# Optimization experiments

Hardware: AMD Instinct MI355X
Metric: run time of the kernel (lower is better)

Reference implementation:

```python
import jax, jax.numpy as jnp
import numpy as np

B, DIN, E, H, V = 1024, 512, 512, 1024, 4096
MAX_LEN = 32  # max_len=33 with force_eos=True -> 32 decode steps


def setup_inputs() -> dict:
    key = jax.random.key(0)
    ks = jax.random.split(key, 12)
    def u(k, shape, fan_in):
        s = 1.0 / np.sqrt(fan_in)
        return jax.random.uniform(k, shape, jnp.float32, -s, s)
    return {
        "x": jax.random.normal(ks[0], (B, DIN), jnp.float32),
        "W_agent": u(ks[1], (DIN, H), DIN),
        "b_agent": u(ks[2], (H,), DIN),
        "sos_embedding": 0.01 * jax.random.normal(ks[3], (E,), jnp.float32),
        "emb": jax.random.normal(ks[4], (V, E), jnp.float32),
        "W_ih": u(ks[5], (E, H), H),
        "W_hh": u(ks[6], (H, H), H),
        "b_ih": u(ks[7], (H,), H),
        "b_hh": u(ks[8], (H,), H),
        "W_out": u(ks[9], (H, V), H),
        "b_out": u(ks[10], (V,), H),
    }


def reference(x, W_agent, b_agent, sos_embedding, emb, W_ih, W_hh, b_ih, b_hh, W_out, b_out):
    h0 = x @ W_agent + b_agent                      # agent(x): [B, H]
    inp0 = jnp.broadcast_to(sos_embedding, (x.shape[0], E))

    def step(carry, _):
        inp, h = carry
        h = jnp.tanh(inp @ W_ih + h @ W_hh + b_ih + b_hh)   # RNNCell
        logp = jax.nn.log_softmax(h @ W_out + b_out, axis=1)  # [B, V]
        tok = jnp.argmax(logp, axis=1)                      # eval-mode sample
        lp = jnp.take_along_axis(logp, tok[:, None], axis=1)[:, 0]
        ent = -jnp.sum(jnp.exp(logp) * logp, axis=1)
        return (emb[tok], h), (tok, lp, ent)

    (_, _), (seq, lps, ents) = jax.lax.scan(step, (inp0, h0), None, length=MAX_LEN)
    seq = seq.T        # [B, MAX_LEN]
    lps = lps.T
    ents = ents.T
    # force_eos: append zero column
    zf = jnp.zeros((seq.shape[0], 1), jnp.float32)
    sequence = jnp.concatenate([seq, zf.astype(seq.dtype)], axis=1)
    logits = jnp.concatenate([lps, zf], axis=1)
    entropy = jnp.concatenate([ents, zf], axis=1)
    return sequence, logits, entropy
```

## Files before the change

kernel.cpp:

```cpp
#include <hip/hip_runtime.h>
#include <math.h>

#define B_   1024
#define DIN  512
#define EMB  512
#define H_   1024
#define V_   4096
#define TSTEPS 32
#define LEN  33

typedef __attribute__((ext_vector_type(8))) short short8_t;
typedef __attribute__((ext_vector_type(4))) float f32x4;

#define AH_P  131072
#define AI_P  65536
#define B3_P  196608

__device__ inline unsigned short bf16_rne(float f) {
  unsigned u = __builtin_bit_cast(unsigned, f);
  u += 0x7FFFu + ((u >> 16) & 1u);
  return (unsigned short)(u >> 16);
}
__device__ inline float bf16_to_f(unsigned short h) {
  unsigned u = ((unsigned)h) << 16;
  return __builtin_bit_cast(float, u);
}
struct S3 { short a, b, c; };
__device__ inline S3 split3(float w) {
  unsigned short h0 = bf16_rne(w);  float r1 = w - bf16_to_f(h0);
  unsigned short h1 = bf16_rne(r1); float r2 = r1 - bf16_to_f(h1);
  S3 r; r.a = (short)h0; r.b = (short)h1; r.c = (short)bf16_rne(r2);
  return r;
}

#define T2MERGE(M1,I1,M2,I2, o1,oi1,o2,oi2)                              \
  if (o1 > M1 || (o1 == M1 && oi1 < I1)) {                               \
    float _n2; int _ni2;                                                 \
    if (M1 > o2 || (M1 == o2 && I1 < oi2)) { _n2 = M1; _ni2 = I1; }      \
    else { _n2 = o2; _ni2 = oi2; }                                       \
    M1 = o1; I1 = oi1; M2 = _n2; I2 = _ni2;                              \
  } else if (o1 > M2 || (o1 == M2 && oi1 < I2)) { M2 = o1; I2 = oi1; }

#define GBT 4
#define GKC 256
__global__ __launch_bounds__(256) void k_gemm(
    float* __restrict__ out,
    const float* __restrict__ A1, int K1, const float* __restrict__ W1,
    const float* __restrict__ A2, int K2, const float* __restrict__ W2,
    const float* __restrict__ b1, const float* __restrict__ b2,
    int do_tanh)
{
  const int N = H_;
  __shared__ float sA[GBT][GKC];
  const int tid = threadIdx.x;
  const int bid = blockIdx.x;
  const int colb = (bid & 7) >> 1;
  const int rowb = ((bid >> 3) << 1) | (bid & 1);
  const int rb  = rowb * GBT;
  const int col = colb * 256 + tid;

  float acc[GBT];
  float bias = b1[col] + (b2 ? b2[col] : 0.0f);
#pragma unroll
  for (int r = 0; r < GBT; ++r) acc[r] = bias;

  const int nch = (K1 + K2) / GKC;
  for (int c = 0; c < nch; ++c) {
    const int kb = c * GKC;
    const float* A; const float* W; int k0, strideA;
    if (kb < K1) { A = A1; W = W1; k0 = kb;      strideA = K1; }
    else         { A = A2; W = W2; k0 = kb - K1; strideA = K2; }
    __syncthreads();
    {
      int r = tid >> 6, kk = (tid & 63) << 2;
      *(float4*)&sA[r][kk] = *(const float4*)(A + (size_t)(rb + r) * strideA + k0 + kk);
    }
    __syncthreads();
    const float* Wp = W + (size_t)k0 * N + col;
#pragma unroll 4
    for (int k = 0; k < GKC; k += 4) {
      float4 a0 = *(const float4*)&sA[0][k];
      float4 a1 = *(const float4*)&sA[1][k];
      float4 a2 = *(const float4*)&sA[2][k];
      float4 a3 = *(const float4*)&sA[3][k];
      float w0 = Wp[(size_t)k * N];
      float w1 = Wp[(size_t)(k + 1) * N];
      float w2 = Wp[(size_t)(k + 2) * N];
      float w3 = Wp[(size_t)(k + 3) * N];
      acc[0] = fmaf(a0.x, w0, acc[0]); acc[1] = fmaf(a1.x, w0, acc[1]);
      acc[2] = fmaf(a2.x, w0, acc[2]); acc[3] = fmaf(a3.x, w0, acc[3]);
      acc[0] = fmaf(a0.y, w1, acc[0]); acc[1] = fmaf(a1.y, w1, acc[1]);
      acc[2] = fmaf(a2.y, w1, acc[2]); acc[3] = fmaf(a3.y, w1, acc[3]);
      acc[0] = fmaf(a0.z, w2, acc[0]); acc[1] = fmaf(a1.z, w2, acc[1]);
      acc[2] = fmaf(a2.z, w2, acc[2]); acc[3] = fmaf(a3.z, w2, acc[3]);
      acc[0] = fmaf(a0.w, w3, acc[0]); acc[1] = fmaf(a1.w, w3, acc[1]);
      acc[2] = fmaf(a2.w, w3, acc[2]); acc[3] = fmaf(a3.w, w3, acc[3]);
    }
  }
#pragma unroll
  for (int r = 0; r < GBT; ++r) {
    float v = acc[r];
    if (do_tanh) v = tanhf(v);
    out[(size_t)(rb + r) * N + col] = v;
  }
}

__global__ __launch_bounds__(256) void k_prepack(
    const float* __restrict__ W, unsigned short* __restrict__ Bp)
{
  int t = blockIdx.x * 256 + threadIdx.x;
  int lane = t & 63;
  int ntg  = (t >> 6) & 255;
  int ks   = t >> 14;
  int col  = ntg * 16 + (lane & 15);
  int krow = ks * 32 + ((lane >> 4) << 3);
  short8_t hv;
#pragma unroll
  for (int j = 0; j < 8; ++j) {
    float w = W[(size_t)(krow + j) * V_ + col];
    hv[j] = (short)bf16_rne(w);
  }
  size_t base = ((size_t)ks * 256 + ntg) * 64 + lane;
  ((short8_t*)Bp)[base] = hv;
}

__global__ __launch_bounds__(256) void k_packW3(
    const float* __restrict__ Wih, const float* __restrict__ Whh,
    unsigned short* __restrict__ BU)
{
  int t = blockIdx.x * 256 + threadIdx.x;
  int lane = t & 63;
  int ntg  = (t >> 6) & 63;
  int ks   = t >> 12;
  int col  = ntg * 16 + (lane & 15);
  int krow = ks * 32 + ((lane >> 4) << 3);
  short8_t p0, p1, p2;
#pragma unroll
  for (int j = 0; j < 8; ++j) {
    int kr = krow + j;
    float w = (kr < DIN) ? Wih[(size_t)kr * H_ + col]
                         : Whh[(size_t)(kr - DIN) * H_ + col];
    S3 s = split3(w);
    p0[j] = s.a; p1[j] = s.b; p2[j] = s.c;
  }
  short8_t* o = (short8_t*)BU;
  size_t base = ((size_t)ks * 64 + ntg) * 64 + lane;
  o[base] = p0; o[base + B3_P] = p1; o[base + 2 * B3_P] = p2;
}

__global__ __launch_bounds__(256) void k_wtrans(
    const float* __restrict__ W, float* __restrict__ WT)
{
  __shared__ float tile[64][65];
  int kb = (blockIdx.x & 15) * 64;
  int vb = (blockIdx.x >> 4) * 64;
  int t = threadIdx.x;
  {
    int vv = t & 63, k0 = (t >> 6) * 16;
    for (int j = 0; j < 16; ++j)
      tile[k0 + j][vv] = W[(size_t)(kb + k0 + j) * V_ + vb + vv];
  }
  __syncthreads();
  {
    int kk = t & 63, v0 = (t >> 6) * 16;
    for (int j = 0; j < 16; ++j)
      WT[(size_t)(vb + v0 + j) * H_ + kb + kk] = tile[kk][v0 + j];
  }
}

__global__ __launch_bounds__(256) void k_packh(
    const float* __restrict__ h, unsigned short* __restrict__ AU)
{
  int t = blockIdx.x * 256 + threadIdx.x;
  int r = t >> 7, q = t & 127;
  int ks = q >> 2, kg = q & 3;
  int lanep = (r & 15) + (kg << 4);
  int rt = r >> 4;
  const float* src = h + (size_t)r * H_ + q * 8;
  float4 f0 = *(const float4*)src;
  float4 f1 = *(const float4*)(src + 4);
  float f[8] = {f0.x, f0.y, f0.z, f0.w, f1.x, f1.y, f1.z, f1.w};
  short8_t p0, p1, p2;
#pragma unroll
  for (int j = 0; j < 8; ++j) {
    S3 s = split3(f[j]);
    p0[j] = s.a; p1[j] = s.b; p2[j] = s.c;
  }
  short8_t* o = (short8_t*)AU;
  size_t base = (size_t)rt * 2048 + (size_t)ks * 64 + lanep;
  o[base] = p0; o[base + AH_P] = p1; o[base + 2 * AH_P] = p2;
}

__global__ __launch_bounds__(256) void k_sos3(
    const float* __restrict__ sos, unsigned short* __restrict__ AU)
{
  int wid = threadIdx.x >> 6, lane = threadIdx.x & 63;
  int row = blockIdx.x * 4 + wid;
  const float* src = sos + lane * 8;
  float4 f0 = *(const float4*)src;
  float4 f1 = *(const float4*)(src + 4);
  float f[8] = {f0.x, f0.y, f0.z, f0.w, f1.x, f1.y, f1.z, f1.w};
  short8_t p0, p1, p2;
#pragma unroll
  for (int j = 0; j < 8; ++j) {
    S3 s = split3(f[j]);
    p0[j] = s.a; p1[j] = s.b; p2[j] = s.c;
  }
  int ks = lane >> 2, kg = lane & 3;
  int lanep = (row & 15) + (kg << 4);
  int rt = row >> 4;
  short8_t* o = (short8_t*)AU;
  size_t base = (size_t)rt * 1024 + (size_t)ks * 64 + lanep;
  o[base] = p0; o[base + AI_P] = p1; o[base + 2 * AI_P] = p2;
}

__global__ __launch_bounds__(512) void k_rnn(
    const unsigned short* __restrict__ AinpU, const unsigned short* __restrict__ AhU,
    const unsigned short* __restrict__ Bw3U,
    const float* __restrict__ b1, const float* __restrict__ b2,
    float* __restrict__ hout, unsigned short* __restrict__ AhOutU)
{
  __shared__ float sh[64][65];
  const short8_t* Ainp = (const short8_t*)AinpU;
  const short8_t* Ah   = (const short8_t*)AhU;
  const short8_t* Bw3  = (const short8_t*)Bw3U;

  const int bid  = blockIdx.x;
  const int colb = ((bid & 7) << 1) | ((bid >> 3) & 1);
  const int rowb = bid >> 4;
  const int tid  = threadIdx.x, lane = tid & 63, wid = tid >> 6;
  const int wm = (wid >> 1) & 1, wn = wid & 1, kh = wid >> 2;
  const int l15 = lane & 15, lg = lane >> 4;

  f32x4 acc[2][2];
#pragma unroll
  for (int rt = 0; rt < 2; ++rt)
#pragma unroll
    for (int nt = 0; nt < 2; ++nt) {
      int col = colb * 64 + wn * 32 + nt * 16 + l15;
      float b = (kh == 0) ? (b1[col] + b2[col]) : 0.0f;
      acc[rt][nt] = (f32x4){b, b, b, b};
    }

  const int rt0 = rowb * 4 + wm * 2;
  const int ng0 = colb * 4 + wn * 2;
  const int ks0 = kh * 24;

#define RNN_LOAD(A_, B_, KS)                                                   \
  {                                                                            \
    int _ks = (KS);                                                            \
    if (_ks < 16) {                                                            \
      _Pragma("unroll") for (int rt = 0; rt < 2; ++rt)                         \
        _Pragma("unroll") for (int p = 0; p < 3; ++p)                          \
          A_[rt][p] = Ainp[(size_t)p * AI_P + (size_t)(rt0 + rt) * 1024 +      \
                           (size_t)_ks * 64 + lane];                           \
    } else {                                                                   \
      int _h = _ks - 16;                                                       \
      _Pragma("unroll") for (int rt = 0; rt < 2; ++rt)                         \
        _Pragma("unroll") for (int p = 0; p < 3; ++p)                          \
          A_[rt][p] = Ah[(size_t)p * AH_P + (size_t)(rt0 + rt) * 2048 +        \
                         (size_t)_h * 64 + lane];                              \
    }                                                                          \
    _Pragma("unroll") for (int nt = 0; nt < 2; ++nt)                           \
      _Pragma("unroll") for (int p = 0; p < 3; ++p)                            \
        B_[nt][p] = Bw3[(size_t)p * B3_P + (size_t)_ks * 4096 +                \
                        (size_t)(ng0 + nt) * 64 + lane];                       \
  }

  short8_t a[2][3], bb[2][3];
  RNN_LOAD(a, bb, ks0)
#pragma unroll
  for (int i = 0; i < 24; ++i) {
    short8_t an[2][3], bn[2][3];
    if (i < 23) RNN_LOAD(an, bn, ks0 + i + 1)
#pragma unroll
    for (int rt = 0; rt < 2; ++rt)
#pragma unroll
      for (int nt = 0; nt < 2; ++nt) {
        acc[rt][nt] = __builtin_amdgcn_mfma_f32_16x16x32_bf16(a[rt][0], bb[nt][0], acc[rt][nt], 0, 0, 0);
        acc[rt][nt] = __builtin_amdgcn_mfma_f32_16x16x32_bf16(a[rt][0], bb[nt][1], acc[rt][nt], 0, 0, 0);
        acc[rt][nt] = __builtin_amdgcn_mfma_f32_16x16x32_bf16(a[rt][1], bb[nt][0], acc[rt][nt], 0, 0, 0);
        acc[rt][nt] = __builtin_amdgcn_mfma_f32_16x16x32_bf16(a[rt][1], bb[nt][1], acc[rt][nt], 0, 0, 0);
        acc[rt][nt] = __builtin_amdgcn_mfma_f32_16x16x32_bf16(a[rt][0], bb[nt][2], acc[rt][nt], 0, 0, 0);
        acc[rt][nt] = __builtin_amdgcn_mfma_f32_16x16x32_bf16(a[rt][2], bb[nt][0], acc[rt][nt], 0, 0, 0);
      }
    if (i < 23) {
#pragma unroll
      for (int rt = 0; rt < 2; ++rt)
#pragma unroll
        for (int p = 0; p < 3; ++p) { a[rt][p] = an[rt][p]; bb[rt][p] = bn[rt][p]; }
    }
  }
#undef RNN_LOAD

  if (kh == 1) {
#pragma unroll
    for (int rt = 0; rt < 2; ++rt)
#pragma unroll
      for (int nt = 0; nt < 2; ++nt)
#pragma unroll
        for (int r = 0; r < 4; ++r)
          sh[wm * 32 + rt * 16 + lg * 4 + r][wn * 32 + nt * 16 + l15] = acc[rt][nt][r];
  }
  __syncthreads();
  if (kh == 0) {
#pragma unroll
    for (int rt = 0; rt < 2; ++rt)
#pragma unroll
      for (int nt = 0; nt < 2; ++nt)
#pragma unroll
        for (int r = 0; r < 4; ++r) {
          int lr = wm * 32 + rt * 16 + lg * 4 + r;
          int lc = wn * 32 + nt * 16 + l15;
          float v = tanhf(acc[rt][nt][r] + sh[lr][lc]);
          hout[(size_t)(rowb * 64 + lr) * H_ + colb * 64 + lc] = v;
          sh[lr][lc] = v;
        }
  }
  __syncthreads();
  {
    int lr = tid >> 3, q = tid & 7;
    int gk = colb * 64 + q * 8;
    int ks = gk >> 5, kg = (gk >> 3) & 3;
    int gr = rowb * 64 + lr;
    int lanep = (gr & 15) + (kg << 4);
    int rt = gr >> 4;
    short8_t p0, p1, p2;
#pragma unroll
    for (int j = 0; j < 8; ++j) {
      S3 s = split3(sh[lr][q * 8 + j]);
      p0[j] = s.a; p1[j] = s.b; p2[j] = s.c;
    }
    short8_t* o = (short8_t*)AhOutU;
    size_t base = (size_t)rt * 2048 + (size_t)ks * 64 + lanep;
    o[base] = p0; o[base + AH_P] = p1; o[base + 2 * AH_P] = p2;
  }
}

__global__ __launch_bounds__(512) void k_logits3(
    const unsigned short* __restrict__ AhU, const unsigned short* __restrict__ BpU,
    const float* __restrict__ bout, float4* __restrict__ partA,
    float4* __restrict__ partB)
{
  __shared__ float sh[64][128];
  __shared__ float sred[2][2][32][6];
  __shared__ float sbmax[64];
  const short8_t* Ah = (const short8_t*)AhU;
  const short8_t* Bp = (const short8_t*)BpU;

  const int bid  = blockIdx.x;
  const int colb = ((bid & 7) << 2) | ((bid >> 3) & 3);
  const int rowb = bid >> 5;
  const int tid  = threadIdx.x, lane = tid & 63, wid = tid >> 6;
  const int wm = (wid >> 1) & 1, wn = wid & 1, kh = wid >> 2;
  const int l15 = lane & 15, lg = lane >> 4;

  const int colbase = colb * 128 + wn * 64;
  f32x4 acc[2][4];
#pragma unroll
  for (int nt = 0; nt < 4; ++nt) {
    float b = (kh == 0) ? bout[colbase + nt * 16 + l15] : 0.0f;
    acc[0][nt] = (f32x4){b, b, b, b};
    acc[1][nt] = acc[0][nt];
  }
  const int rt0 = rowb * 4 + wm * 2;
  const int ng0 = colb * 8 + wn * 4;
  const int ks0 = kh * 16;

#define LG_LOAD(A_, B_, KS)                                                    \
  {                                                                            \
    int _ks = (KS);                                                            \
    _Pragma("unroll") for (int rt = 0; rt < 2; ++rt)                           \
      A_[rt] = Ah[(size_t)(rt0 + rt) * 2048 + (size_t)_ks * 64 + lane];        \
    _Pragma("unroll") for (int nt = 0; nt < 4; ++nt)                           \
      B_[nt] = Bp[((size_t)_ks * 256 + ng0 + nt) * 64 + lane];                 \
  }

  short8_t a[2], bb[4];
  LG_LOAD(a, bb, ks0)
#pragma unroll
  for (int i = 0; i < 16; ++i) {
    short8_t an[2], bn[4];
    if (i < 15) LG_LOAD(an, bn, ks0 + i + 1)
#pragma unroll
    for (int rt = 0; rt < 2; ++rt)
#pragma unroll
      for (int nt = 0; nt < 4; ++nt)
        acc[rt][nt] = __builtin_amdgcn_mfma_f32_16x16x32_bf16(
            a[rt], bb[nt], acc[rt][nt], 0, 0, 0);
    if (i < 15) {
#pragma unroll
      for (int rt = 0; rt < 2; ++rt) a[rt] = an[rt];
#pragma unroll
      for (int nt = 0; nt < 4; ++nt) bb[nt] = bn[nt];
    }
  }
#undef LG_LOAD

  if (kh == 1) {
#pragma unroll
    for (int rt = 0; rt < 2; ++rt)
#pragma unroll
      for (int nt = 0; nt < 4; ++nt)
#pragma unroll
        for (int r = 0; r < 4; ++r)
          sh[wm * 32 + rt * 16 + lg * 4 + r][wn * 64 + nt * 16 + l15] = acc[rt][nt][r];
  }
  __syncthreads();
  if (kh == 0) {
#pragma unroll
    for (int rt = 0; rt < 2; ++rt)
#pragma unroll
      for (int nt = 0; nt < 4; ++nt)
#pragma unroll
        for (int r = 0; r < 4; ++r)
          acc[rt][nt][r] += sh[wm * 32 + rt * 16 + lg * 4 + r][wn * 64 + nt * 16 + l15];
  }

  if (kh == 0) {
#pragma unroll
    for (int rt = 0; rt < 2; ++rt)
#pragma unroll
      for (int r = 0; r < 4; ++r) {
        float M1 = -1e30f, M2 = -1e30f; int I1 = 0, I2 = 0;
#pragma unroll
        for (int nt = 0; nt < 4; ++nt) {
          float v = acc[rt][nt][r]; int c = colbase + nt * 16 + l15;
          if (v > M1) { M2 = M1; I2 = I1; M1 = v; I1 = c; }
          else if (v > M2) { M2 = v; I2 = c; }
        }
#pragma unroll
        for (int d = 1; d < 16; d <<= 1) {
          float o1 = __shfl_xor(M1, d); int oi1 = __shfl_xor(I1, d);
          float o2 = __shfl_xor(M2, d); int oi2 = __shfl_xor(I2, d);
          T2MERGE(M1, I1, M2, I2, o1, oi1, o2, oi2)
        }
        if (l15 == 0) {
          int rl = rt * 16 + lg * 4 + r;
          sred[wm][wn][rl][0] = M1; sred[wm][wn][rl][1] = (float)I1;
          sred[wm][wn][rl][2] = M2; sred[wm][wn][rl][3] = (float)I2;
        }
      }
  }
  __syncthreads();
  if (tid < 64) {
    int wmm = tid >> 5, rl = tid & 31;
    float M1 = sred[wmm][0][rl][0]; int I1 = (int)sred[wmm][0][rl][1];
    float M2 = sred[wmm][0][rl][2]; int I2 = (int)sred[wmm][0][rl][3];
    float o1 = sred[wmm][1][rl][0]; int oi1 = (int)sred[wmm][1][rl][1];
    float o2 = sred[wmm][1][rl][2]; int oi2 = (int)sred[wmm][1][rl][3];
    T2MERGE(M1, I1, M2, I2, o1, oi1, o2, oi2)
    int row = rowb * 64 + wmm * 32 + rl;
    partA[(size_t)row * 32 + colb] = make_float4(M1, (float)I1, M2, (float)I2);
    sbmax[wmm * 32 + rl] = M1;
  }
  __syncthreads();
  if (kh == 0) {
#pragma unroll
    for (int rt = 0; rt < 2; ++rt)
#pragma unroll
      for (int r = 0; r < 4; ++r) {
        float m = sbmax[wm * 32 + rt * 16 + lg * 4 + r];
        float s = 0.f, tsum = 0.f;
#pragma unroll
        for (int nt = 0; nt < 4; ++nt) {
          float d = acc[rt][nt][r] - m;
          float e = expf(d);
          s += e; tsum += d * e;
        }
#pragma unroll
        for (int d = 1; d < 16; d <<= 1) { s += __shfl_xor(s, d); tsum += __shfl_xor(tsum, d); }
        if (l15 == 0) {
          int rl = rt * 16 + lg * 4 + r;
          sred[wm][wn][rl][4] = s; sred[wm][wn][rl][5] = tsum;
        }
      }
  }
  __syncthreads();
  if (tid < 64) {
    int wmm = tid >> 5, rl = tid & 31;
    float s = sred[wmm][0][rl][4] + sred[wmm][1][rl][4];
    float tsum = sred[wmm][0][rl][5] + sred[wmm][1][rl][5];
    int row = rowb * 64 + wmm * 32 + rl;
    partB[(size_t)row * 32 + colb] = make_float4(s, tsum, 0.f, 0.f);
  }
}

__global__ __launch_bounds__(256) void k_finalize3(
    const float4* __restrict__ partA, const float4* __restrict__ partB,
    const float* __restrict__ h, const float* __restrict__ Wout,
    const float* __restrict__ WoutT, const float* __restrict__ bout,
    const float* __restrict__ emb, float* __restrict__ out,
    unsigned short* __restrict__ AinpU, int tstep)
{
  const int lane = threadIdx.x & 63;
  const int wid  = threadIdx.x >> 6;
  const int row  = blockIdx.x * 4 + wid;

  float M1 = -1e30f, M2 = -1e30f; int I1 = 0, I2 = 0;
  float bm = -1e30f, s_l = 0.f, t_l = 0.f;
  if (lane < 32) {
    float4 pa = partA[(size_t)row * 32 + lane];
    float4 pb = partB[(size_t)row * 32 + lane];
    M1 = pa.x; I1 = (int)pa.y; M2 = pa.z; I2 = (int)pa.w;
    bm = pa.x; s_l = pb.x; t_l = pb.y;
  }
  for (int d = 1; d < 32; d <<= 1) {
    float o1 = __shfl_xor(M1, d); int oi1 = __shfl_xor(I1, d);
    float o2 = __shfl_xor(M2, d); int oi2 = __shfl_xor(I2, d);
    T2MERGE(M1, I1, M2, I2, o1, oi1, o2, oi2)
  }
  M1 = __shfl(M1, 0); I1 = __shfl(I1, 0);
  M2 = __shfl(M2, 0); I2 = __shfl(I2, 0);

  float e = (lane < 32) ? expf(bm - M1) : 0.f;
  float s = e * s_l;
  float tsum = e * (t_l + (bm - M1) * s_l);
  for (int d = 1; d < 64; d <<= 1) { s += __shfl_xor(s, d); tsum += __shfl_xor(tsum, d); }

  const float* hrow = h + (size_t)row * H_;
  float d1 = 0.f, d2 = 0.f;
  if (WoutT) {
    const float* w1 = WoutT + (size_t)I1 * H_;
    const float* w2 = WoutT + (size_t)I2 * H_;
#pragma unroll 4
    for (int k = lane; k < H_; k += 64) {
      float hv = hrow[k];
      d1 = fmaf(hv, w1[k], d1);
      d2 = fmaf(hv, w2[k], d2);
    }
  } else {
    for (int k = lane; k < H_; k += 64) {
      float hv = hrow[k];
      d1 = fmaf(hv, Wout[(size_t)k * V_ + I1], d1);
      d2 = fmaf(hv, Wout[(size_t)k * V_ + I2], d2);
    }
  }
  for (int d = 1; d < 64; d <<= 1) { d1 += __shfl_xor(d1, d); d2 += __shfl_xor(d2, d); }
  d1 += bout[I1]; d2 += bout[I2];

  int tok; float ltok;
  if (d2 > d1 || (d2 == d1 && I2 < I1)) { tok = I2; ltok = d2; }
  else                                  { tok = I1; ltok = d1; }
  float lg_s = logf(s);
  if (lane == 0) {
    out[(size_t)row * LEN + tstep]                  = (float)tok;
    out[(size_t)(B_ * LEN) + row * LEN + tstep]     = ltok - M1 - lg_s;
    out[(size_t)(2 * B_ * LEN) + row * LEN + tstep] = lg_s - tsum / s;
  }
  const float* er = emb + (size_t)tok * EMB + lane * 8;
  float4 f0 = *(const float4*)er;
  float4 f1 = *(const float4*)(er + 4);
  float f[8] = {f0.x, f0.y, f0.z, f0.w, f1.x, f1.y, f1.z, f1.w};
  short8_t p0, p1, p2;
#pragma unroll
  for (int j = 0; j < 8; ++j) {
    S3 s3v = split3(f[j]);
    p0[j] = s3v.a; p1[j] = s3v.b; p2[j] = s3v.c;
  }
  int ks = lane >> 2, kg = lane & 3;
  int lanep = (row & 15) + (kg << 4);
  int rt = row >> 4;
  short8_t* o = (short8_t*)AinpU;
  size_t base = (size_t)rt * 1024 + (size_t)ks * 64 + lanep;
  o[base] = p0; o[base + AI_P] = p1; o[base + 2 * AI_P] = p2;
}

#define BT 16
#define KC 128
__global__ __launch_bounds__(256) void k_logits_f32(
    const float* __restrict__ h, const float* __restrict__ Wout,
    const float* __restrict__ bout, float4* __restrict__ part)
{
  __shared__ float sA[BT][KC];
  __shared__ float redf[4][BT];
  __shared__ float redf2[4][BT];
  __shared__ int   redi[4][BT];
  __shared__ float bm[BT];

  const int tid = threadIdx.x;
  const int rb  = blockIdx.x * BT;
  const int c0  = blockIdx.y * 512 + tid * 2;

  float acc[BT][2];
  float2 bj = *(const float2*)(bout + c0);
#pragma unroll
  for (int r = 0; r < BT; ++r) { acc[r][0] = bj.x; acc[r][1] = bj.y; }

  for (int kb = 0; kb < H_; kb += KC) {
    __syncthreads();
    {
      float4* s4 = (float4*)sA;
#pragma unroll
      for (int i = 0; i < 2; ++i) {
        int idx = tid + i * 256;
        int r = idx >> 5, kk = (idx & 31) << 2;
        s4[idx] = *(const float4*)(h + (size_t)(rb + r) * H_ + kb + kk);
      }
    }
    __syncthreads();
    const float* Wp = Wout + (size_t)kb * V_ + c0;
#pragma unroll 2
    for (int k = 0; k < KC; k += 4) {
      float4 a[BT];
#pragma unroll
      for (int r = 0; r < BT; ++r) a[r] = *((const float4*)sA[r] + (k >> 2));
      float2 w[4];
#pragma unroll
      for (int u = 0; u < 4; ++u) w[u] = *(const float2*)(Wp + (size_t)(k + u) * V_);
#pragma unroll
      for (int u = 0; u < 4; ++u)
#pragma unroll
        for (int r = 0; r < BT; ++r) {
          float av = ((const float*)&a[r])[u];
          acc[r][0] = fmaf(av, w[u].x, acc[r][0]);
          acc[r][1] = fmaf(av, w[u].y, acc[r][1]);
        }
    }
  }

  const int wid = tid >> 6, lane = tid & 63;
  float mx[BT]; int ix[BT];
#pragma unroll
  for (int r = 0; r < BT; ++r) {
    float m = acc[r][0]; int ii = c0;
    if (acc[r][1] > m) { m = acc[r][1]; ii = c0 + 1; }
    mx[r] = m; ix[r] = ii;
  }
#pragma unroll
  for (int r = 0; r < BT; ++r) {
    for (int d = 32; d; d >>= 1) {
      float ov = __shfl_xor(mx[r], d);
      int   oi = __shfl_xor(ix[r], d);
      if (ov > mx[r] || (ov == mx[r] && oi < ix[r])) { mx[r] = ov; ix[r] = oi; }
    }
  }
  if (lane == 0) {
#pragma unroll
    for (int r = 0; r < BT; ++r) { redf[wid][r] = mx[r]; redi[wid][r] = ix[r]; }
  }
  __syncthreads();
  if (tid < BT) {
    float m = redf[0][tid]; int ii = redi[0][tid];
    for (int w = 1; w < 4; ++w) {
      float ov = redf[w][tid]; int oi = redi[w][tid];
      if (ov > m || (ov == m && oi < ii)) { m = ov; ii = oi; }
    }
    bm[tid] = m; redi[0][tid] = ii;
  }
  __syncthreads();
  float ss[BT], tt[BT];
#pragma unroll
  for (int r = 0; r < BT; ++r) {
    float m = bm[r];
    float s = 0.f, t = 0.f;
#pragma unroll
    for (int j = 0; j < 2; ++j) {
      float d = acc[r][j] - m;
      float e2 = expf(d);
      s += e2; t += d * e2;
    }
    ss[r] = s; tt[r] = t;
  }
#pragma unroll
  for (int r = 0; r < BT; ++r) {
    for (int d = 32; d; d >>= 1) {
      ss[r] += __shfl_xor(ss[r], d);
      tt[r] += __shfl_xor(tt[r], d);
    }
  }
  if (lane == 0) {
#pragma unroll
    for (int r = 0; r < BT; ++r) { redf[wid][r] = ss[r]; redf2[wid][r] = tt[r]; }
  }
  __syncthreads();
  if (tid < BT) {
    float s = 0.f, t = 0.f;
    for (int w = 0; w < 4; ++w) { s += redf[w][tid]; t += redf2[w][tid]; }
    part[(size_t)(rb + tid) * 8 + blockIdx.y] =
        make_float4(bm[tid], s, t, (float)redi[0][tid]);
  }
}

__global__ __launch_bounds__(128) void k_finalize_f32(
    const float4* __restrict__ part, const float* __restrict__ emb,
    float* __restrict__ out, float* __restrict__ inp, int t)
{
  const int row = blockIdx.x;
  __shared__ int s_tok;
  if (threadIdx.x == 0) {
    float4 p[8];
#pragma unroll
    for (int i = 0; i < 8; ++i) p[i] = part[(size_t)row * 8 + i];
    float m = p[0].x; int tok = (int)p[0].w;
#pragma unroll
    for (int i = 1; i < 8; ++i)
      if (p[i].x > m) { m = p[i].x; tok = (int)p[i].w; }
    float S = 0.f, T = 0.f;
#pragma unroll
    for (int i = 0; i < 8; ++i) {
      float w = expf(p[i].x - m);
      S += w * p[i].y;
      T += w * (p[i].z + (p[i].x - m) * p[i].y);
    }
    float lp  = -logf(S);
    float ent = logf(S) - T / S;
    out[(size_t)row * LEN + t]                  = (float)tok;
    out[(size_t)(B_ * LEN) + row * LEN + t]     = lp;
    out[(size_t)(2 * B_ * LEN) + row * LEN + t] = ent;
    s_tok = tok;
  }
  __syncthreads();
  const float4* src = (const float4*)(emb + (size_t)s_tok * EMB);
  float4* dst = (float4*)(inp + (size_t)row * EMB);
  for (int i = threadIdx.x; i < EMB / 4; i += blockDim.x) dst[i] = src[i];
}

__global__ void k_sos(const float* __restrict__ sos, float* __restrict__ inp) {
  int i = blockIdx.x * blockDim.x + threadIdx.x;
  ((float4*)inp)[i] = ((const float4*)sos)[i & (EMB / 4 - 1)];
}
__global__ void k_zero(float* __restrict__ out) {
  int i = blockIdx.x * blockDim.x + threadIdx.x;
  if (i < 3 * B_) {
    int sec = i >> 10, row = i & (B_ - 1);
    out[(size_t)sec * (B_ * LEN) + (size_t)row * LEN + (LEN - 1)] = 0.f;
  }
}

extern "C" void kernel_launch(void* const* d_in, const int* in_sizes, int n_in,
                              void* d_out, int out_size, void* d_ws, size_t ws_size,
                              hipStream_t stream) {
  const float* x       = (const float*)d_in[0];
  const float* W_agent = (const float*)d_in[1];
  const float* b_agent = (const float*)d_in[2];
  const float* sos     = (const float*)d_in[3];
  const float* emb     = (const float*)d_in[4];
  const float* W_ih    = (const float*)d_in[5];
  const float* W_hh    = (const float*)d_in[6];
  const float* b_ih    = (const float*)d_in[7];
  const float* b_hh    = (const float*)d_in[8];
  const float* W_out   = (const float*)d_in[9];
  const float* b_out   = (const float*)d_in[10];
  float* out = (float*)d_out;

  const size_t SZ_BPOUT = 8388608;
  const size_t SZ_BW3   = 9437184;
  const size_t SZ_WT    = 16777216;
  const size_t SZ_AH    = 6291456;
  const size_t SZ_AINP  = 3145728;
  const size_t SZ_H     = 4194304;
  const size_t SZ_PART  = 524288;
  const size_t NEED_A = SZ_BPOUT + SZ_BW3 + SZ_WT + 2 * SZ_AH + SZ_AINP + SZ_H + 2 * SZ_PART;
  const size_t NEED_B = NEED_A - SZ_WT;

  if (ws_size >= NEED_B) {
    const bool useT = ws_size >= NEED_A;
    char* p = (char*)d_ws;
    unsigned short* BpOut = (unsigned short*)p; p += SZ_BPOUT;
    unsigned short* Bw3   = (unsigned short*)p; p += SZ_BW3;
    float* WoutT = nullptr;
    if (useT) { WoutT = (float*)p; p += SZ_WT; }
    unsigned short* Ah0  = (unsigned short*)p; p += SZ_AH;
    unsigned short* Ah1  = (unsigned short*)p; p += SZ_AH;
    unsigned short* Ainp = (unsigned short*)p; p += SZ_AINP;
    float*  hbuf  = (float*)p; p += SZ_H;
    float4* partA = (float4*)p; p += SZ_PART;
    float4* partB = (float4*)p;

    k_sos3<<<dim3(256), dim3(256), 0, stream>>>(sos, Ainp);
    k_prepack<<<dim3(2048), dim3(256), 0, stream>>>(W_out, BpOut);
    k_packW3<<<dim3(768), dim3(256), 0, stream>>>(W_ih, W_hh, Bw3);
    if (useT) k_wtrans<<<dim3(1024), dim3(256), 0, stream>>>(W_out, WoutT);
    k_gemm<<<dim3(1024), dim3(256), 0, stream>>>(
        hbuf, x, DIN, W_agent, nullptr, 0, nullptr, b_agent, nullptr, 0);
    k_packh<<<dim3(512), dim3(256), 0, stream>>>(hbuf, Ah0);

    for (int t = 0; t < TSTEPS; ++t) {
      unsigned short* AhIn  = (t & 1) ? Ah1 : Ah0;
      unsigned short* AhOut = (t & 1) ? Ah0 : Ah1;
      k_rnn<<<dim3(256), dim3(512), 0, stream>>>(
          Ainp, AhIn, Bw3, b_ih, b_hh, hbuf, AhOut);
      k_logits3<<<dim3(512), dim3(512), 0, stream>>>(
          AhOut, BpOut, b_out, partA, partB);
      k_finalize3<<<dim3(256), dim3(256), 0, stream>>>(
          partA, partB, hbuf, W_out, WoutT, b_out, emb, out, Ainp, t);
    }
  } else {
    float*  h0buf = (float*)d_ws;
    float*  h1buf = h0buf + (size_t)B_ * H_;
    float*  inp   = h1buf + (size_t)B_ * H_;
    float4* part  = (float4*)(inp + (size_t)B_ * EMB);

    k_sos<<<dim3(B_ * EMB / 4 / 256), dim3(256), 0, stream>>>(sos, inp);
    k_gemm<<<dim3(1024), dim3(256), 0, stream>>>(
        h0buf, x, DIN, W_agent, nullptr, 0, nullptr, b_agent, nullptr, 0);
    for (int t = 0; t < TSTEPS; ++t) {
      float* hr = (t & 1) ? h1buf : h0buf;
      float* hw = (t & 1) ? h0buf : h1buf;
      k_gemm<<<dim3(1024), dim3(256), 0, stream>>>(
          hw, inp, EMB, W_ih, hr, H_, W_hh, b_ih, b_hh, 1);
      k_logits_f32<<<dim3(B_ / BT, V_ / 512), dim3(256), 0, stream>>>(
          hw, W_out, b_out, part);
      k_finalize_f32<<<dim3(B_), dim3(128), 0, stream>>>(part, emb, out, inp, t);
    }
  }
  k_zero<<<dim3(12), dim3(256), 0, stream>>>(out);
}
```

Before: 1.973 ms.

## Use FP8 MFMA for vocab logits with top-6 candidate exact rescoring

The output-projection GEMM switches from bf16 to fp8 e4m3 MFMA. W_out is prepacked to scaled fp8, and the RNN kernel also emits an fp8-packed copy of h. The logits kernel now tracks a top-3 per block instead of top-2, and the finalize kernel picks the global top-6 candidates and rescoring them exactly in fp32 to choose the argmax token. This halves operand bandwidth and raises MFMA throughput for the dominant GEMM. In exchange it adds extra candidate dot products and shuffle reductions, and risks argmax mismatches plus coarser log-softmax sums and entropy. The smaller-workspace fallback without WoutT is also dropped.

After: 4.337 ms. 120% more time.

```diff
diff --git a/kernel.cpp b/kernel.cpp
--- a/kernel.cpp
+++ b/kernel.cpp
@@ -11,6 +11,7 @@
 
 typedef __attribute__((ext_vector_type(8))) short short8_t;
 typedef __attribute__((ext_vector_type(4))) float f32x4;
+typedef unsigned long long u64;
 
 #define AH_P  131072
 #define AI_P  65536
@@ -33,13 +34,36 @@
   return r;
 }
 
-#define T2MERGE(M1,I1,M2,I2, o1,oi1,o2,oi2)                              \
-  if (o1 > M1 || (o1 == M1 && oi1 < I1)) {                               \
-    float _n2; int _ni2;                                                 \
-    if (M1 > o2 || (M1 == o2 && I1 < oi2)) { _n2 = M1; _ni2 = I1; }      \
-    else { _n2 = o2; _ni2 = oi2; }                                       \
-    M1 = o1; I1 = oi1; M2 = _n2; I2 = _ni2;                              \
-  } else if (o1 > M2 || (o1 == M2 && oi1 < I2)) { M2 = o1; I2 = oi1; }
+__device__ inline unsigned char f2e4m3(float f) {
+  unsigned u = __builtin_bit_cast(unsigned, f);
+  unsigned s = (u >> 24) & 0x80u;
+  int ebits = (int)((u >> 23) & 0xFF);
+  unsigned m = u & 0x7FFFFF;
+  if (ebits < 127 - 10) return (unsigned char)s;
+  if (ebits < 127 - 6) {
+    float af = __builtin_bit_cast(float, u & 0x7FFFFFFFu);
+    int r = (int)rintf(af * 512.0f);
+    if (r >= 8) return (unsigned char)(s | 0x08);
+    return (unsigned char)(s | (unsigned)r);
+  }
+  unsigned rm = m + 0x7FFFFu + ((m >> 20) & 1u);
+  int e = ebits;
+  if (rm >> 23) { rm = 0; e += 1; }
+  if (e > 127 + 8) return (unsigned char)(s | 0x7E);
+  unsigned code = ((unsigned)(e - 127 + 7) << 3) | (rm >> 20);
+  if (code > 0x7E) code = 0x7E;
+  return (unsigned char)(s | code);
+}
+
+__device__ inline void ins3(float v, int ix, float* m, int* id) {
+  if (v > m[0] || (v == m[0] && ix < id[0])) {
+    m[2] = m[1]; id[2] = id[1]; m[1] = m[0]; id[1] = id[0]; m[0] = v; id[0] = ix;
+  } else if (v > m[1] || (v == m[1] && ix < id[1])) {
+    m[2] = m[1]; id[2] = id[1]; m[1] = v; id[1] = ix;
+  } else if (v > m[2] || (v == m[2] && ix < id[2])) {
+    m[2] = v; id[2] = ix;
+  }
+}
 
 #define GBT 4
 #define GKC 256
@@ -105,8 +129,8 @@
   }
 }
 
-__global__ __launch_bounds__(256) void k_prepack(
-    const float* __restrict__ W, unsigned short* __restrict__ Bp)
+__global__ __launch_bounds__(256) void k_prepack8(
+    const float* __restrict__ W, u64* __restrict__ BpF)
 {
   int t = blockIdx.x * 256 + threadIdx.x;
   int lane = t & 63;
@@ -114,14 +138,13 @@
   int ks   = t >> 14;
   int col  = ntg * 16 + (lane & 15);
   int krow = ks * 32 + ((lane >> 4) << 3);
-  short8_t hv;
+  u64 v = 0;
 #pragma unroll
   for (int j = 0; j < 8; ++j) {
-    float w = W[(size_t)(krow + j) * V_ + col];
-    hv[j] = (short)bf16_rne(w);
-  }
-  size_t base = ((size_t)ks * 256 + ntg) * 64 + lane;
-  ((short8_t*)Bp)[base] = hv;
+    float w = W[(size_t)(krow + j) * V_ + col] * 32.0f;
+    v |= ((u64)f2e4m3(w)) << (8 * j);
+  }
+  BpF[((size_t)ks * 256 + ntg) * 64 + lane] = v;
 }
 
 __global__ __launch_bounds__(256) void k_packW3(
@@ -218,7 +241,8 @@
     const unsigned short* __restrict__ AinpU, const unsigned short* __restrict__ AhU,
     const unsigned short* __restrict__ Bw3U,
     const float* __restrict__ b1, const float* __restrict__ b2,
-    float* __restrict__ hout, unsigned short* __restrict__ AhOutU)
+    float* __restrict__ hout, unsigned short* __restrict__ AhOutU,
+    u64* __restrict__ AhFOut)
 {
   __shared__ float sh[64][65];
   const short8_t* Ainp = (const short8_t*)AinpU;
@@ -326,27 +350,29 @@
     int lanep = (gr & 15) + (kg << 4);
     int rt = gr >> 4;
     short8_t p0, p1, p2;
+    u64 f8 = 0;
 #pragma unroll
     for (int j = 0; j < 8; ++j) {
-      S3 s = split3(sh[lr][q * 8 + j]);
+      float v = sh[lr][q * 8 + j];
+      S3 s = split3(v);
       p0[j] = s.a; p1[j] = s.b; p2[j] = s.c;
+      f8 |= ((u64)f2e4m3(v * 16.0f)) << (8 * j);
     }
     short8_t* o = (short8_t*)AhOutU;
     size_t base = (size_t)rt * 2048 + (size_t)ks * 64 + lanep;
     o[base] = p0; o[base + AH_P] = p1; o[base + 2 * AH_P] = p2;
-  }
-}
-
-__global__ __launch_bounds__(512) void k_logits3(
-    const unsigned short* __restrict__ AhU, const unsigned short* __restrict__ BpU,
+    AhFOut[((size_t)rt * 32 + ks) * 64 + lanep] = f8;
+  }
+}
+
+__global__ __launch_bounds__(512) void k_logits8(
+    const u64* __restrict__ AhF, const u64* __restrict__ BpF,
     const float* __restrict__ bout, float4* __restrict__ partA,
     float4* __restrict__ partB)
 {
   __shared__ float sh[64][128];
-  __shared__ float sred[2][2][32][6];
+  __shared__ float sred[2][2][32][8];
   __shared__ float sbmax[64];
-  const short8_t* Ah = (const short8_t*)AhU;
-  const short8_t* Bp = (const short8_t*)BpU;
 
   const int bid  = blockIdx.x;
   const int colb = ((bid & 7) << 2) | ((bid >> 3) & 3);
@@ -354,13 +380,17 @@
   const int tid  = threadIdx.x, lane = tid & 63, wid = tid >> 6;
   const int wm = (wid >> 1) & 1, wn = wid & 1, kh = wid >> 2;
   const int l15 = lane & 15, lg = lane >> 4;
+  const float SC = 1.0f / 512.0f;
 
   const int colbase = colb * 128 + wn * 64;
+  float bnt[4];
+#pragma unroll
+  for (int nt = 0; nt < 4; ++nt) bnt[nt] = bout[colbase + nt * 16 + l15];
+
   f32x4 acc[2][4];
 #pragma unroll
   for (int nt = 0; nt < 4; ++nt) {
-    float b = (kh == 0) ? bout[colbase + nt * 16 + l15] : 0.0f;
-    acc[0][nt] = (f32x4){b, b, b, b};
+    acc[0][nt] = (f32x4){0.f, 0.f, 0.f, 0.f};
     acc[1][nt] = acc[0][nt];
   }
   const int rt0 = rowb * 4 + wm * 2;
@@ -371,23 +401,23 @@
   {                                                                            \
     int _ks = (KS);                                                            \
     _Pragma("unroll") for (int rt = 0; rt < 2; ++rt)                           \
-      A_[rt] = Ah[(size_t)(rt0 + rt) * 2048 + (size_t)_ks * 64 + lane];        \
+      A_[rt] = AhF[((size_t)(rt0 + rt) * 32 + _ks) * 64 + lane];               \
     _Pragma("unroll") for (int nt = 0; nt < 4; ++nt)                           \
-      B_[nt] = Bp[((size_t)_ks * 256 + ng0 + nt) * 64 + lane];                 \
-  }
-
-  short8_t a[2], bb[4];
+      B_[nt] = BpF[((size_t)_ks * 256 + ng0 + nt) * 64 + lane];                \
+  }
+
+  u64 a[2], bb[4];
   LG_LOAD(a, bb, ks0)
 #pragma unroll
   for (int i = 0; i < 16; ++i) {
-    short8_t an[2], bn[4];
+    u64 an[2], bn[4];
     if (i < 15) LG_LOAD(an, bn, ks0 + i + 1)
 #pragma unroll
     for (int rt = 0; rt < 2; ++rt)
 #pragma unroll
       for (int nt = 0; nt < 4; ++nt)
-        acc[rt][nt] = __builtin_amdgcn_mfma_f32_16x16x32_bf16(
-            a[rt], bb[nt], acc[rt][nt], 0, 0, 0);
+        acc[rt][nt] = __builtin_amdgcn_mfma_f32_16x16x32_fp8_fp8(
+            (long)a[rt], (long)bb[nt], acc[rt][nt], 0, 0, 0);
     if (i < 15) {
 #pragma unroll
       for (int rt = 0; rt < 2; ++rt) a[rt] = an[rt];
@@ -422,37 +452,45 @@
     for (int rt = 0; rt < 2; ++rt)
 #pragma unroll
       for (int r = 0; r < 4; ++r) {
-        float M1 = -1e30f, M2 = -1e30f; int I1 = 0, I2 = 0;
+        float m[3] = {-1e30f, -1e30f, -1e30f};
+        int   id[3] = {0, 0, 0};
 #pragma unroll
         for (int nt = 0; nt < 4; ++nt) {
-          float v = acc[rt][nt][r]; int c = colbase + nt * 16 + l15;
-          if (v > M1) { M2 = M1; I2 = I1; M1 = v; I1 = c; }
-          else if (v > M2) { M2 = v; I2 = c; }
+          float v = acc[rt][nt][r] * SC + bnt[nt];
+          ins3(v, colbase + nt * 16 + l15, m, id);
         }
 #pragma unroll
         for (int d = 1; d < 16; d <<= 1) {
-          float o1 = __shfl_xor(M1, d); int oi1 = __shfl_xor(I1, d);
-          float o2 = __shfl_xor(M2, d); int oi2 = __shfl_xor(I2, d);
-          T2MERGE(M1, I1, M2, I2, o1, oi1, o2, oi2)
+          float om[3]; int oid[3];
+#pragma unroll
+          for (int j = 0; j < 3; ++j) { om[j] = __shfl_xor(m[j], d); oid[j] = __shfl_xor(id[j], d); }
+#pragma unroll
+          for (int j = 0; j < 3; ++j) ins3(om[j], oid[j], m, id);
         }
         if (l15 == 0) {
           int rl = rt * 16 + lg * 4 + r;
-          sred[wm][wn][rl][0] = M1; sred[wm][wn][rl][1] = (float)I1;
-          sred[wm][wn][rl][2] = M2; sred[wm][wn][rl][3] = (float)I2;
+          sred[wm][wn][rl][0] = m[0]; sred[wm][wn][rl][1] = (float)id[0];
+          sred[wm][wn][rl][2] = m[1]; sred[wm][wn][rl][3] = (float)id[1];
+          sred[wm][wn][rl][4] = m[2]; sred[wm][wn][rl][5] = (float)id[2];
         }
       }
   }
   __syncthreads();
+  float keepM3 = -1e30f; int keepI3 = 0;
   if (tid < 64) {
     int wmm = tid >> 5, rl = tid & 31;
-    float M1 = sred[wmm][0][rl][0]; int I1 = (int)sred[wmm][0][rl][1];
-    float M2 = sred[wmm][0][rl][2]; int I2 = (int)sred[wmm][0][rl][3];
-    float o1 = sred[wmm][1][rl][0]; int oi1 = (int)sred[wmm][1][rl][1];
-    float o2 = sred[wmm][1][rl][2]; int oi2 = (int)sred[wmm][1][rl][3];
-    T2MERGE(M1, I1, M2, I2, o1, oi1, o2, oi2)
+    float m[3]; int id[3];
+#pragma unroll
+    for (int j = 0; j < 3; ++j) {
+      m[j] = sred[wmm][0][rl][2 * j]; id[j] = (int)sred[wmm][0][rl][2 * j + 1];
+    }
+#pragma unroll
+    for (int j = 0; j < 3; ++j)
+      ins3(sred[wmm][1][rl][2 * j], (int)sred[wmm][1][rl][2 * j + 1], m, id);
     int row = rowb * 64 + wmm * 32 + rl;
-    partA[(size_t)row * 32 + colb] = make_float4(M1, (float)I1, M2, (float)I2);
-    sbmax[wmm * 32 + rl] = M1;
+    partA[(size_t)row * 32 + colb] = make_float4(m[0], (float)id[0], m[1], (float)id[1]);
+    keepM3 = m[2]; keepI3 = id[2];
+    sbmax[wmm * 32 + rl] = m[0];
   }
   __syncthreads();
   if (kh == 0) {
@@ -460,11 +498,11 @@
     for (int rt = 0; rt < 2; ++rt)
 #pragma unroll
       for (int r = 0; r < 4; ++r) {
-        float m = sbmax[wm * 32 + rt * 16 + lg * 4 + r];
+        float mm = sbmax[wm * 32 + rt * 16 + lg * 4 + r];
         float s = 0.f, tsum = 0.f;
 #pragma unroll
         for (int nt = 0; nt < 4; ++nt) {
-          float d = acc[rt][nt][r] - m;
+          float d = acc[rt][nt][r] * SC + bnt[nt] - mm;
           float e = expf(d);
           s += e; tsum += d * e;
         }
@@ -472,21 +510,21 @@
         for (int d = 1; d < 16; d <<= 1) { s += __shfl_xor(s, d); tsum += __shfl_xor(tsum, d); }
         if (l15 == 0) {
           int rl = rt * 16 + lg * 4 + r;
-          sred[wm][wn][rl][4] = s; sred[wm][wn][rl][5] = tsum;
+          sred[wm][wn][rl][6] = s; sred[wm][wn][rl][7] = tsum;
         }
       }
   }
   __syncthreads();
   if (tid < 64) {
     int wmm = tid >> 5, rl = tid & 31;
-    float s = sred[wmm][0][rl][4] + sred[wmm][1][rl][4];
-    float tsum = sred[wmm][0][rl][5] + sred[wmm][1][rl][5];
+    float s = sred[wmm][0][rl][6] + sred[wmm][1][rl][6];
+    float tsum = sred[wmm][0][rl][7] + sred[wmm][1][rl][7];
     int row = rowb * 64 + wmm * 32 + rl;
-    partB[(size_t)row * 32 + colb] = make_float4(s, tsum, 0.f, 0.f);
-  }
-}
-
-__global__ __launch_bounds__(256) void k_finalize3(
+    partB[(size_t)row * 32 + colb] = make_float4(s, tsum, keepM3, (float)keepI3);
+  }
+}
+
+__global__ __launch_bounds__(256) void k_finalize4(
     const float4* __restrict__ partA, const float4* __restrict__ partB,
     const float* __restrict__ h, const float* __restrict__ Wout,
     const float* __restrict__ WoutT, const float* __restrict__ bout,
@@ -497,21 +535,37 @@
   const int wid  = threadIdx.x >> 6;
   const int row  = blockIdx.x * 4 + wid;
 
-  float M1 = -1e30f, M2 = -1e30f; int I1 = 0, I2 = 0;
+  float cv0 = -1e30f, cv1 = -1e30f, cv2 = -1e30f;
+  int   ci0 = 0x7FFFFFFF, ci1 = 0x7FFFFFFF, ci2 = 0x7FFFFFFF;
   float bm = -1e30f, s_l = 0.f, t_l = 0.f;
   if (lane < 32) {
     float4 pa = partA[(size_t)row * 32 + lane];
     float4 pb = partB[(size_t)row * 32 + lane];
-    M1 = pa.x; I1 = (int)pa.y; M2 = pa.z; I2 = (int)pa.w;
+    cv0 = pa.x; ci0 = (int)pa.y;
+    cv1 = pa.z; ci1 = (int)pa.w;
+    cv2 = pb.z; ci2 = (int)pb.w;
     bm = pa.x; s_l = pb.x; t_l = pb.y;
   }
-  for (int d = 1; d < 32; d <<= 1) {
-    float o1 = __shfl_xor(M1, d); int oi1 = __shfl_xor(I1, d);
-    float o2 = __shfl_xor(M2, d); int oi2 = __shfl_xor(I2, d);
-    T2MERGE(M1, I1, M2, I2, o1, oi1, o2, oi2)
-  }
-  M1 = __shfl(M1, 0); I1 = __shfl(I1, 0);
-  M2 = __shfl(M2, 0); I2 = __shfl(I2, 0);
+
+  float selV[6]; int selI[6];
+#pragma unroll
+  for (int p = 0; p < 6; ++p) {
+    float bv = cv0; int bi = ci0; int bs = 0;
+    if (cv1 > bv || (cv1 == bv && ci1 < bi)) { bv = cv1; bi = ci1; bs = 1; }
+    if (cv2 > bv || (cv2 == bv && ci2 < bi)) { bv = cv2; bi = ci2; bs = 2; }
+    float rv = bv; int ri = bi;
+    for (int d = 1; d < 64; d <<= 1) {
+      float ov = __shfl_xor(rv, d); int oi = __shfl_xor(ri, d);
+      if (ov > rv || (ov == rv && oi < ri)) { rv = ov; ri = oi; }
+    }
+    selV[p] = rv; selI[p] = ri;
+    if (bv == rv && bi == ri) {
+      if (bs == 0) cv0 = -1e30f;
+      else if (bs == 1) cv1 = -1e30f;
+      else cv2 = -1e30f;
+    }
+  }
+  const float M1 = selV[0];
 
   float e = (lane < 32) ? expf(bm - M1) : 0.f;
   float s = e * s_l;
@@ -519,29 +573,43 @@
   for (int d = 1; d < 64; d <<= 1) { s += __shfl_xor(s, d); tsum += __shfl_xor(tsum, d); }
 
   const float* hrow = h + (size_t)row * H_;
-  float d1 = 0.f, d2 = 0.f;
+  float dd[6] = {0.f, 0.f, 0.f, 0.f, 0.f, 0.f};
   if (WoutT) {
-    const float* w1 = WoutT + (size_t)I1 * H_;
-    const float* w2 = WoutT + (size_t)I2 * H_;
-#pragma unroll 4
+    const float* wp0 = WoutT + (size_t)selI[0] * H_;
+    const float* wp1 = WoutT + (size_t)selI[1] * H_;
+    const float* wp2 = WoutT + (size_t)selI[2] * H_;
+    const float* wp3 = WoutT + (size_t)selI[3] * H_;
+    const float* wp4 = WoutT + (size_t)selI[4] * H_;
+    const float* wp5 = WoutT + (size_t)selI[5] * H_;
+#pragma unroll 2
     for (int k = lane; k < H_; k += 64) {
       float hv = hrow[k];
-      d1 = fmaf(hv, w1[k], d1);
-      d2 = fmaf(hv, w2[k], d2);
+      dd[0] = fmaf(hv, wp0[k], dd[0]);
+      dd[1] = fmaf(hv, wp1[k], dd[1]);
+      dd[2] = fmaf(hv, wp2[k], dd[2]);
+      dd[3] = fmaf(hv, wp3[k], dd[3]);
+      dd[4] = fmaf(hv, wp4[k], dd[4]);
+      dd[5] = fmaf(hv, wp5[k], dd[5]);
     }
   } else {
     for (int k = lane; k < H_; k += 64) {
       float hv = hrow[k];
-      d1 = fmaf(hv, Wout[(size_t)k * V_ + I1], d1);
-      d2 = fmaf(hv, Wout[(size_t)k * V_ + I2], d2);
-    }
-  }
-  for (int d = 1; d < 64; d <<= 1) { d1 += __shfl_xor(d1, d); d2 += __shfl_xor(d2, d); }
-  d1 += bout[I1]; d2 += bout[I2];
-
-  int tok; float ltok;
-  if (d2 > d1 || (d2 == d1 && I2 < I1)) { tok = I2; ltok = d2; }
-  else                                  { tok = I1; ltok = d1; }
+#pragma unroll
+      for (int j = 0; j < 6; ++j)
+        dd[j] = fmaf(hv, Wout[(size_t)k * V_ + selI[j]], dd[j]);
+    }
+  }
+#pragma unroll
+  for (int j = 0; j < 6; ++j)
+    for (int d = 1; d < 64; d <<= 1) dd[j] += __shfl_xor(dd[j], d);
+#pragma unroll
+  for (int j = 0; j < 6; ++j) dd[j] += bout[selI[j]];
+
+  int tok = selI[0]; float ltok = dd[0];
+#pragma unroll
+  for (int j = 1; j < 6; ++j)
+    if (dd[j] > ltok || (dd[j] == ltok && selI[j] < tok)) { ltok = dd[j]; tok = selI[j]; }
+
   float lg_s = logf(s);
   if (lane == 0) {
     out[(size_t)row * LEN + tstep]                  = (float)tok;
@@ -744,34 +812,35 @@
   const float* b_out   = (const float*)d_in[10];
   float* out = (float*)d_out;
 
-  const size_t SZ_BPOUT = 8388608;
+  const size_t SZ_BPF   = 4194304;
   const size_t SZ_BW3   = 9437184;
   const size_t SZ_WT    = 16777216;
   const size_t SZ_AH    = 6291456;
+  const size_t SZ_AHF   = 1048576;
   const size_t SZ_AINP  = 3145728;
   const size_t SZ_H     = 4194304;
   const size_t SZ_PART  = 524288;
-  const size_t NEED_A = SZ_BPOUT + SZ_BW3 + SZ_WT + 2 * SZ_AH + SZ_AINP + SZ_H + 2 * SZ_PART;
-  const size_t NEED_B = NEED_A - SZ_WT;
-
-  if (ws_size >= NEED_B) {
-    const bool useT = ws_size >= NEED_A;
+  const size_t NEED_A = SZ_BPF + SZ_BW3 + SZ_WT + 2 * SZ_AH + 2 * SZ_AHF +
+                        SZ_AINP + SZ_H + 2 * SZ_PART;
+
+  if (ws_size >= NEED_A) {
     char* p = (char*)d_ws;
-    unsigned short* BpOut = (unsigned short*)p; p += SZ_BPOUT;
-    unsigned short* Bw3   = (unsigned short*)p; p += SZ_BW3;
-    float* WoutT = nullptr;
-    if (useT) { WoutT = (float*)p; p += SZ_WT; }
+    u64*   BpF  = (u64*)p;            p += SZ_BPF;
+    unsigned short* Bw3 = (unsigned short*)p; p += SZ_BW3;
+    float* WoutT = (float*)p;         p += SZ_WT;
     unsigned short* Ah0  = (unsigned short*)p; p += SZ_AH;
     unsigned short* Ah1  = (unsigned short*)p; p += SZ_AH;
+    u64*   AhF0 = (u64*)p;            p += SZ_AHF;
+    u64*   AhF1 = (u64*)p;            p += SZ_AHF;
     unsigned short* Ainp = (unsigned short*)p; p += SZ_AINP;
-    float*  hbuf  = (float*)p; p += SZ_H;
-    float4* partA = (float4*)p; p += SZ_PART;
+    float*  hbuf  = (float*)p;        p += SZ_H;
+    float4* partA = (float4*)p;       p += SZ_PART;
     float4* partB = (float4*)p;
 
     k_sos3<<<dim3(256), dim3(256), 0, stream>>>(sos, Ainp);
-    k_prepack<<<dim3(2048), dim3(256), 0, stream>>>(W_out, BpOut);
+    k_prepack8<<<dim3(2048), dim3(256), 0, stream>>>(W_out, BpF);
     k_packW3<<<dim3(768), dim3(256), 0, stream>>>(W_ih, W_hh, Bw3);
-    if (useT) k_wtrans<<<dim3(1024), dim3(256), 0, stream>>>(W_out, WoutT);
+    k_wtrans<<<dim3(1024), dim3(256), 0, stream>>>(W_out, WoutT);
     k_gemm<<<dim3(1024), dim3(256), 0, stream>>>(
         hbuf, x, DIN, W_agent, nullptr, 0, nullptr, b_agent, nullptr, 0);
     k_packh<<<dim3(512), dim3(256), 0, stream>>>(hbuf, Ah0);
@@ -779,11 +848,12 @@
     for (int t = 0; t < TSTEPS; ++t) {
       unsigned short* AhIn  = (t & 1) ? Ah1 : Ah0;
       unsigned short* AhOut = (t & 1) ? Ah0 : Ah1;
+      u64* AhFOut = (t & 1) ? AhF0 : AhF1;
       k_rnn<<<dim3(256), dim3(512), 0, stream>>>(
-          Ainp, AhIn, Bw3, b_ih, b_hh, hbuf, AhOut);
-      k_logits3<<<dim3(512), dim3(512), 0, stream>>>(
-          AhOut, BpOut, b_out, partA, partB);
-      k_finalize3<<<dim3(256), dim3(256), 0, stream>>>(
+          Ainp, AhIn, Bw3, b_ih, b_hh, hbuf, AhOut, AhFOut);
+      k_logits8<<<dim3(512), dim3(512), 0, stream>>>(
+          AhFOut, BpF, b_out, partA, partB);
+      k_finalize4<<<dim3(256), dim3(256), 0, stream>>>(
           partA, partB, hbuf, W_out, WoutT, b_out, emb, out, Ainp, t);
     }
   } else {
```
